# Optimization experiments

Measured on AMD Instinct MI355X. Metric: run time of the kernel, lower is better.

The kernel has to match this reference:

```python
import jax, jax.numpy as jnp
from jax import lax
import numpy as np

B = 2048; D_IN = 784; H = 256; N_OUT = 10

def setup_inputs() -> dict:
    key = jax.random.key(0)
    ks = jax.random.split(key, 12)
    return {
        "x": jax.random.uniform(ks[0], (B, D_IN), jnp.float32),
        "h1": jax.random.randint(ks[1], (B, H), 0, 2, jnp.int32),
        "h2": jax.random.randint(ks[2], (B, H), 0, 2, jnp.int32),
        "y": jax.random.randint(ks[3], (B, N_OUT), 0, 2, jnp.int32),
        "W1": jax.random.normal(ks[4], (D_IN, H), jnp.float32) * 0.05,
        "b1": jnp.zeros((H,), jnp.float32),
        "W2": jax.random.normal(ks[5], (H, H), jnp.float32) * 0.05,
        "b2": jnp.zeros((H,), jnp.float32),
        "Wout": jax.random.normal(ks[6], (H, N_OUT), jnp.float32) * 0.05,
        "bout": jnp.zeros((N_OUT,), jnp.float32),
        # pre-drawn per-node Bernoulli uniforms, shape [H, B] (scan axis first)
        "u1": jax.random.uniform(ks[7], (H, B), jnp.float32),
        "u2": jax.random.uniform(ks[8], (H, B), jnp.float32),
    }

def _sigmoid_ce(labels, logits):
    # tf.nn.sigmoid_cross_entropy_with_logits, numerically stable
    return jnp.maximum(logits, 0.0) - logits * labels + jnp.log1p(jnp.exp(-jnp.abs(logits)))

def _gibbs_layer(pv, cv, nv, W_in, b_in, W_out, b_out, u):
    """One layer of node-by-node Gibbs resampling.
    pv: [B, P] parents, cv: [B, H] current layer (old values),
    nv: [B, Hn] children, u: [H, B] uniforms. Returns (new cv [B,H], final child logits [B,Hn])."""
    parent_logits = pv @ W_in + b_in          # [B, H]; sigmoid(.) = prob_parents
    next_logits0 = cv @ W_out + b_out         # [B, Hn], recurrently updated

    def step(nl, xs):
        node, w_j, pl_j, u_j = xs             # [B], [Hn], [B], [B]
        nl0 = nl - node[:, None] * w_j[None, :]
        nl1 = nl + (1.0 - node)[:, None] * w_j[None, :]
        lp0 = -jnp.sum(_sigmoid_ce(nv, nl0), axis=-1)
        lp1 = -jnp.sum(_sigmoid_ce(nv, nl1), axis=-1)
        # prob = p1/(p1+p0) with p1 = sigm(pl)*exp(lp1), p0 = (1-sigm(pl))*exp(lp0)
        # == sigmoid(pl + lp1 - lp0)  (same math, stable form)
        prob = jax.nn.sigmoid(pl_j + lp1 - lp0)
        new = (u_j < prob).astype(jnp.float32)
        nl_new = jnp.where(new[:, None] > 0.5, nl1, nl0)
        return nl_new, new

    nl_fin, new_T = lax.scan(step, next_logits0, (cv.T, W_out, parent_logits.T, u))
    return new_T.T, nl_fin

def reference(x, h1, h2, y, W1, b1, W2, b2, Wout, bout, u1, u2):
    h1f = h1.astype(jnp.float32)
    h2f = h2.astype(jnp.float32)
    yf = y.astype(jnp.float32)
    # layer 0: parents=x, children=h2 (old values)
    h1_new, _ = _gibbs_layer(x, h1f, h2f, W1, b1, W2, b2, u1)
    # layer 1: parents=h1_new (already updated), children=y, out layer = output_layer
    h2_new, nl_fin = _gibbs_layer(h1_new, h2f, yf, W2, b2, Wout, bout, u2)
    # pack new states + final output-layer logits into one array [B, H+H+N_OUT]
    return jnp.concatenate([h1_new, h2_new, nl_fin], axis=1)
```

## Files before the change

kernel.cpp:

```cpp
#include <hip/hip_runtime.h>
#include <math.h>

#define NB   2048
#define DIN  784
#define HN   256
#define NOUT 10
#define OSTR (HN + HN + NOUT)

struct Smem {
  float4  sup[4][HN];
  double2 tab[65];
  float   scr[4][16 * 20];
  float   h2o[4][HN];
  float   h1n[4][HN];
  float   tmp[4][HN];
  float   yv [4][16];
};

__device__ __forceinline__ float np_expf(float xf) {
  float q = __fmul_rn(xf, 1.442695040888963f);
  q = __fadd_rn(q, 12582912.0f);
  q = __fsub_rn(q, 12582912.0f);
  float x = __builtin_fmaf(q, -6.93145752e-1f, xf);
  x = __builtin_fmaf(q, -1.42860677e-6f, x);
  float num = __builtin_fmaf(x, 5.082762527590693718096e-04f,
                                6.757896990527504603057e-03f);
  num = __builtin_fmaf(num, x, 5.114512081637298353406e-02f);
  num = __builtin_fmaf(num, x, 2.473615434895520810817e-01f);
  num = __builtin_fmaf(num, x, 7.257664613233124478488e-01f);
  num = __builtin_fmaf(num, x, 9.999999999980870924916e-01f);
  float den = __builtin_fmaf(x, 2.159509375685829852307e-02f,
                                -2.742335390411667452936e-01f);
  den = __builtin_fmaf(den, x, 1.0f);
  float r = __fdiv_rn(num, den);
  int qi = (int)q;
  return __fmul_rn(r, __int_as_float((qi + 127) << 23));
}

__device__ __forceinline__ float np_log1pf(float ef, const double2* __restrict__ tab) {
  if (ef < 0x1p-29f) return ef;
  double t  = 1.0 + (double)ef;
  double kd = rint(t * 64.0);
  int   idx = (int)kd - 64;
  double2 te = tab[idx];
  double c  = kd * 0.015625;
  double s  = (t - c) * te.y;
  double p  = fma(s, -1.0/6.0, 0.2);
  p = fma(p, s, -0.25);
  p = fma(p, s,  1.0/3.0);
  p = fma(p, s, -0.5);
  p = fma(p, s,  1.0);
  p = p * s;
  return (float)(te.x + p);
}

__device__ __forceinline__ float ce32(float l, float label, const double2* __restrict__ tab) {
  float t3 = __fsub_rn(fmaxf(l, 0.0f), __fmul_rn(l, label));
  return __fadd_rn(t3, np_log1pf(np_expf(-fabsf(l)), tab));
}

__device__ __forceinline__ bool decide(float u, float ez) {
  float w = __fadd_rn(1.0f, ez);
  float d = __builtin_fmaf(u, w, -1.0f);
  if (__builtin_expect(fabsf(d) < 1e-5f, 0)) {
    float prob = __fdiv_rn(1.0f, w);
    return u < prob;
  }
  return d < 0.0f;
}

template<int CTRL> __device__ __forceinline__ float dppx(float v) {
  return __int_as_float(__builtin_amdgcn_mov_dpp(__float_as_int(v), CTRL, 0xF, 0xF, true));
}
__device__ __forceinline__ float rdl(float v, int l) {
  return __int_as_float(__builtin_amdgcn_readlane(__float_as_int(v), l));
}

__device__ __forceinline__ float sum10(float c) {
  float c0 = rdl(c, 0), c1 = rdl(c, 1), c2 = rdl(c, 2), c3 = rdl(c, 3);
  float c4 = rdl(c, 4), c5 = rdl(c, 5), c6 = rdl(c, 6), c7 = rdl(c, 7);
  float c8 = rdl(c, 8), c9 = rdl(c, 9);
  float t = __fadd_rn(__fadd_rn(__fadd_rn(c0, c1), __fadd_rn(c2, c3)),
                      __fadd_rn(__fadd_rn(c4, c5), __fadd_rn(c6, c7)));
  t = __fadd_rn(t, c8);
  t = __fadd_rn(t, c9);
  return t;
}

__device__ __forceinline__ float fold256_lds(const float c[4], float* __restrict__ scrw,
                                             int idx, int g) {
  *reinterpret_cast<float4*>(scrw + idx * 20 + 4 * g) = make_float4(c[0], c[1], c[2], c[3]);
  const float4* rp = reinterpret_cast<const float4*>(scrw + idx * 20);
  float4 q0 = rp[0], q1 = rp[1], q2 = rp[2], q3 = rp[3];
  float r = q0.x;
  r = __fadd_rn(r, q0.y); r = __fadd_rn(r, q0.z); r = __fadd_rn(r, q0.w);
  r = __fadd_rn(r, q1.x); r = __fadd_rn(r, q1.y); r = __fadd_rn(r, q1.z); r = __fadd_rn(r, q1.w);
  r = __fadd_rn(r, q2.x); r = __fadd_rn(r, q2.y); r = __fadd_rn(r, q2.z); r = __fadd_rn(r, q2.w);
  r = __fadd_rn(r, q3.x); r = __fadd_rn(r, q3.y); r = __fadd_rn(r, q3.z); r = __fadd_rn(r, q3.w);
  r = __fadd_rn(r, dppx<0xB1>(r));
  r = __fadd_rn(r, dppx<0x4E>(r));
  float B0 = rdl(r, 0), B1 = rdl(r, 4), B2 = rdl(r, 8), B3 = rdl(r, 12);
  return __fadd_rn(__fadd_rn(B0, B1), __fadd_rn(B2, B3));
}

__device__ __forceinline__ float fast_sum256(float loc) {
  float r = loc;
  r = r + dppx<0xB1>(r);
  r = r + dppx<0x4E>(r);
  r = r + dppx<0x124>(r);
  r = r + dppx<0x128>(r);
  r = r + dppx<0x142>(r);
  r = r + dppx<0x143>(r);
  return rdl(r, 63);
}

__device__ __forceinline__ float lu_of(float u) {
  if (u < 1e-4f || u > 0.9999f) return __int_as_float(0x7FC00000);
  return __logf(u) - __logf(__fsub_rn(1.0f, u));
}

#define ZBAND 0.05f
#define LN2F  0.6931471805599453f

__global__ __launch_bounds__(256) void stoch_mlp(
    const float* __restrict__ x,  const int* __restrict__ h1,
    const int* __restrict__ h2,   const int* __restrict__ y,
    const float* __restrict__ W1, const float* __restrict__ b1,
    const float* __restrict__ W2, const float* __restrict__ b2,
    const float* __restrict__ Wo, const float* __restrict__ bo,
    const float* __restrict__ u1, const float* __restrict__ u2,
    float* __restrict__ out)
{
  __shared__ Smem sm;
  const int t    = threadIdx.x;
  const int lane = t & 63;
  const int wid  = t >> 6;
  const int b0   = blockIdx.x * 4;
  const int b    = b0 + wid;

  if (t < 65) {
    double c = (double)(t + 64) * 0.015625;
    sm.tab[t] = make_double2(log(c), 64.0 / (double)(t + 64));
  }
  for (int j = lane; j < HN; j += 64) sm.h2o[wid][j] = (float)h2[b * HN + j];
  if (lane < 16) sm.yv[wid][lane] = (lane < NOUT) ? (float)y[b * NOUT + lane] : 0.0f;
  {
    float a0 = 0.0f, a1 = 0.0f, a2 = 0.0f, a3 = 0.0f;
    const float* x0 = x + (size_t)b0 * DIN;
    float wk0 = W1[t];
    float wk1 = W1[HN + t];
    for (int k = 0; k < DIN; ++k) {
      int k2 = (k + 2 < DIN) ? (k + 2) : 0;
      float wk2 = W1[(size_t)k2 * HN + t];
      a0 = __builtin_fmaf(x0[k],           wk0, a0);
      a1 = __builtin_fmaf(x0[DIN   + k],   wk0, a1);
      a2 = __builtin_fmaf(x0[2*DIN + k],   wk0, a2);
      a3 = __builtin_fmaf(x0[3*DIN + k],   wk0, a3);
      wk0 = wk1; wk1 = wk2;
    }
    float bb = b1[t];
    float4 uv = *reinterpret_cast<const float4*>(u1 + (size_t)t * NB + b0);
    float n0 = (float)h1[(b0 + 0) * HN + t];
    float n1 = (float)h1[(b0 + 1) * HN + t];
    float n2 = (float)h1[(b0 + 2) * HN + t];
    float n3 = (float)h1[(b0 + 3) * HN + t];
    sm.sup[0][t] = make_float4(n0, uv.x, __fadd_rn(a0, bb), lu_of(uv.x));
    sm.sup[1][t] = make_float4(n1, uv.y, __fadd_rn(a1, bb), lu_of(uv.y));
    sm.sup[2][t] = make_float4(n2, uv.z, __fadd_rn(a2, bb), lu_of(uv.z));
    sm.sup[3][t] = make_float4(n3, uv.w, __fadd_rn(a3, bb), lu_of(uv.w));
  }
  __syncthreads();

  const double2* tab = sm.tab;
  float* scrw = &sm.scr[wid][0];

  {
    float acc[4] = {0.0f, 0.0f, 0.0f, 0.0f};
    for (int j = 0; j < HN; ++j) {
      float nodej = sm.sup[wid][j].x;
      float4 wf = *reinterpret_cast<const float4*>(W2 + (size_t)j * HN + 4*lane);
      acc[0] = __builtin_fmaf(nodej, wf.x, acc[0]);
      acc[1] = __builtin_fmaf(nodej, wf.y, acc[1]);
      acc[2] = __builtin_fmaf(nodej, wf.z, acc[2]);
      acc[3] = __builtin_fmaf(nodej, wf.w, acc[3]);
    }
    float4 bv = *reinterpret_cast<const float4*>(b2 + 4*lane);
    *reinterpret_cast<float4*>(&sm.tmp[wid][4*lane]) =
        make_float4(__fadd_rn(acc[0], bv.x), __fadd_rn(acc[1], bv.y),
                    __fadd_rn(acc[2], bv.z), __fadd_rn(acc[3], bv.w));
  }

  const int idx  = lane & 15;
  const int g    = lane >> 4;
  const int half = idx >> 3;
  const int jacc = idx & 7;
  const int kb   = half * 128 + (4 * g) * 8 + jacc;

  float nlv[4], nv[4];
  int   smk[4];
  #pragma unroll
  for (int i = 0; i < 4; ++i) {
    int k = kb + i * 8;
    nlv[i] = sm.tmp[wid][k];
    nv[i]  = sm.h2o[wid][k];
    smk[i] = (nv[i] != 0.0f) ? (int)0x80000000 : 0;
  }
  float S_c;
  {
    float ci[4];
    #pragma unroll
    for (int i = 0; i < 4; ++i) ci[i] = ce32(nlv[i], nv[i], tab);
    S_c = fold256_lds(ci, scrw, idx, g);
  }

  {
    float4 supC = sm.sup[wid][0];
    float4 supN = sm.sup[wid][1];
    float w0[4], w1[4];
    #pragma unroll
    for (int i = 0; i < 4; ++i) {
      w0[i] = W2[kb + i * 8];
      w1[i] = W2[(size_t)HN + kb + i * 8];
    }
    #pragma unroll 2
    for (int j = 0; j < HN; ++j) {
      int jn2 = (j + 2) & (HN - 1);
      float4 supN2 = sm.sup[wid][jn2];
      float wp[4];
      #pragma unroll
      for (int i = 0; i < 4; ++i) wp[i] = W2[(size_t)jn2 * HN + kb + i * 8];

      float node = supC.x, uj = supC.y, plj = supC.z, luj = supC.w;
      bool  nd   = (node != 0.0f);
      int ndm = nd ? (int)0x80000000 : 0;
      float fresh[4], t3[4], p[4];
      #pragma unroll
      for (int i = 0; i < 4; ++i) {
        float ws = __int_as_float(__float_as_int(w0[i]) ^ ndm);
        fresh[i] = __fadd_rn(nlv[i], ws);
        float sl = __int_as_float(__float_as_int(fresh[i]) ^ smk[i]);
        t3[i] = fmaxf(sl, 0.0f);
        p[i]  = __log2f(__fadd_rn(1.0f, __expf(-fabsf(fresh[i]))));
      }
      float T = (t3[0] + t3[1]) + (t3[2] + t3[3]);
      float P = (p[0]  + p[1])  + (p[2]  + p[3]);
      float F = fast_sum256(__builtin_fmaf(LN2F, P, T));
      float sgn = nd ? 1.0f : -1.0f;
      float z = __builtin_fmaf(F - S_c, sgn, plj);
      float d = z - luj;
      bool nw;
      if (__builtin_expect(!(fabsf(d) >= ZBAND), 0)) {
        float one_m = __fsub_rn(1.0f, node);
        float nl0[4], nl1[4], c0i[4], c1i[4];
        #pragma unroll
        for (int i = 0; i < 4; ++i) {
          nl0[i] = __fsub_rn(nlv[i], __fmul_rn(node,  w0[i]));
          nl1[i] = __fadd_rn(nlv[i], __fmul_rn(one_m, w0[i]));
          c0i[i] = ce32(nl0[i], nv[i], tab);
          c1i[i] = ce32(nl1[i], nv[i], tab);
        }
        float S0e = fold256_lds(c0i, scrw, idx, g);
        float S1e = fold256_lds(c1i, scrw, idx, g);
        float ze  = __fsub_rn(__fadd_rn(plj, -S1e), -S0e);
        nw  = decide(uj, np_expf(-ze));
        S_c = nw ? S1e : S0e;
        #pragma unroll
        for (int i = 0; i < 4; ++i) nlv[i] = nw ? nl1[i] : nl0[i];
      } else {
        nw = d > 0.0f;
        bool flip = (nw != nd);
        S_c = flip ? F : S_c;
        #pragma unroll
        for (int i = 0; i < 4; ++i) nlv[i] = flip ? fresh[i] : nlv[i];
      }
      if (lane == 0) sm.h1n[wid][j] = nw ? 1.0f : 0.0f;
      supC = supN; supN = supN2;
      #pragma unroll
      for (int i = 0; i < 4; ++i) { w0[i] = w1[i]; w1[i] = wp[i]; }
    }
  }

  {
    float acc[4] = {0.0f, 0.0f, 0.0f, 0.0f};
    for (int j = 0; j < HN; ++j) {
      float nodej = sm.h1n[wid][j];
      float4 wf = *reinterpret_cast<const float4*>(W2 + (size_t)j * HN + 4*lane);
      acc[0] = __builtin_fmaf(nodej, wf.x, acc[0]);
      acc[1] = __builtin_fmaf(nodej, wf.y, acc[1]);
      acc[2] = __builtin_fmaf(nodej, wf.z, acc[2]);
      acc[3] = __builtin_fmaf(nodej, wf.w, acc[3]);
    }
    float4 bv = *reinterpret_cast<const float4*>(b2 + 4*lane);
    float p2[4] = {__fadd_rn(acc[0], bv.x), __fadd_rn(acc[1], bv.y),
                   __fadd_rn(acc[2], bv.z), __fadd_rn(acc[3], bv.w)};
    #pragma unroll
    for (int i = 0; i < 4; ++i) {
      int j = 4 * lane + i;
      float u2v = u2[(size_t)j * NB + b];
      sm.sup[wid][j] = make_float4(sm.h2o[wid][j], u2v, p2[i], lu_of(u2v));
    }
  }

  float nvy = 0.0f, nlo = 0.0f;
  if (lane < NOUT) {
    nvy = sm.yv[wid][lane];
    float a = 0.0f;
    for (int j = 0; j < HN; ++j)
      a = __builtin_fmaf(sm.h2o[wid][j], Wo[j * NOUT + lane], a);
    nlo = __fadd_rn(a, bo[lane]);
  }
  float S_c1 = sum10((lane < NOUT) ? ce32(nlo, nvy, tab) : 0.0f);
  const int  syk  = (nvy != 0.0f) ? (int)0x80000000 : 0;
  const bool lact = (lane < NOUT);

  {
    float4 supC = sm.sup[wid][0];
    float4 supN = sm.sup[wid][1];
    float w0s = lact ? Wo[lane] : 0.0f;
    float w1s = lact ? Wo[NOUT + lane] : 0.0f;
    #pragma unroll 2
    for (int j = 0; j < HN; ++j) {
      int jn2 = (j + 2) & (HN - 1);
      float4 supN2 = sm.sup[wid][jn2];
      float wps = lact ? Wo[jn2 * NOUT + lane] : 0.0f;

      float node = supC.x, uj = supC.y, plj = supC.z, luj = supC.w;
      bool  nd   = (node != 0.0f);
      int ndm = nd ? (int)0x80000000 : 0;
      float ws = __int_as_float(__float_as_int(w0s) ^ ndm);
      float fresh = __fadd_rn(nlo, ws);
      float sl = __int_as_float(__float_as_int(fresh) ^ syk);
      float t3 = fmaxf(sl, 0.0f);
      float p  = __log2f(__fadd_rn(1.0f, __expf(-fabsf(fresh))));
      float loc = lact ? __builtin_fmaf(LN2F, p, t3) : 0.0f;
      float r = loc;
      r = r + dppx<0xB1>(r);
      r = r + dppx<0x4E>(r);
      r = r + dppx<0x124>(r);
      r = r + dppx<0x128>(r);
      float F  = rdl(r, 0);
      float sgn = nd ? 1.0f : -1.0f;
      float z = __builtin_fmaf(F - S_c1, sgn, plj);
      float d = z - luj;
      bool nw;
      if (__builtin_expect(!(fabsf(d) >= ZBAND), 0)) {
        float one_m = __fsub_rn(1.0f, node);
        float nl0 = __fsub_rn(nlo, __fmul_rn(node,  w0s));
        float nl1 = __fadd_rn(nlo, __fmul_rn(one_m, w0s));
        float c0 = lact ? ce32(nl0, nvy, tab) : 0.0f;
        float c1 = lact ? ce32(nl1, nvy, tab) : 0.0f;
        float S0e = sum10(c0);
        float S1e = sum10(c1);
        float ze  = __fsub_rn(__fadd_rn(plj, -S1e), -S0e);
        nw   = decide(uj, np_expf(-ze));
        S_c1 = nw ? S1e : S0e;
        nlo  = nw ? nl1 : nl0;
      } else {
        nw = d > 0.0f;
        bool flip = (nw != nd);
        S_c1 = flip ? F : S_c1;
        nlo  = flip ? fresh : nlo;
      }
      if (lane == 0) out[(size_t)b * OSTR + HN + j] = nw ? 1.0f : 0.0f;
      supC = supN; supN = supN2;
      w0s = w1s; w1s = wps;
    }
  }

  float* orow = out + (size_t)b * OSTR;
  for (int j = lane; j < HN; j += 64) orow[j] = sm.h1n[wid][j];
  if (lane < NOUT) orow[2*HN + lane] = nlo;
}

extern "C" void kernel_launch(void* const* d_in, const int* in_sizes, int n_in,
                              void* d_out, int out_size, void* d_ws, size_t ws_size,
                              hipStream_t stream) {
  const float* x  = (const float*)d_in[0];
  const int*   h1 = (const int*)  d_in[1];
  const int*   h2 = (const int*)  d_in[2];
  const int*   y  = (const int*)  d_in[3];
  const float* W1 = (const float*)d_in[4];
  const float* b1 = (const float*)d_in[5];
  const float* W2 = (const float*)d_in[6];
  const float* b2 = (const float*)d_in[7];
  const float* Wo = (const float*)d_in[8];
  const float* bo = (const float*)d_in[9];
  const float* u1 = (const float*)d_in[10];
  const float* u2 = (const float*)d_in[11];
  stoch_mlp<<<NB/4, 256, 0, stream>>>(x, h1, h2, y, W1, b1, W2, b2, Wo, bo, u1, u2,
                                      (float*)d_out);
}
```

Measured before the change: 318.6 us.

## Deepen load prefetch rings and fold node-sign into precomputed decision offset

Replaces the two-deep register prefetch of weights and per-node support data with 4- or 16-deep rotating buffers across the W1, W2, Wo and Gibbs-scan loops, with matching unrolls. The goal is to hide global and LDS load latency in the serial scans. It also precomputes a sign-folded q = ±(pl − logit(u)) per node, so the decision becomes (F − S) + q. It multiplies the four softplus arguments before taking one log2 instead of four. The deeper buffers raise register pressure, and the product-of-logs change slightly alters rounding near the decision band.

```diff
diff --git a/kernel.cpp b/kernel.cpp
--- a/kernel.cpp
+++ b/kernel.cpp
@@ -118,6 +118,11 @@
   if (u < 1e-4f || u > 0.9999f) return __int_as_float(0x7FC00000);
   return __logf(u) - __logf(__fsub_rn(1.0f, u));
 }
+__device__ __forceinline__ float q_of(float node, float pl, float u) {
+  float lu = lu_of(u);
+  float pq = __fsub_rn(pl, lu);
+  return (node != 0.0f) ? pq : -pq;
+}
 
 #define ZBAND 0.05f
 #define LN2F  0.6931471805599453f
@@ -147,16 +152,18 @@
   {
     float a0 = 0.0f, a1 = 0.0f, a2 = 0.0f, a3 = 0.0f;
     const float* x0 = x + (size_t)b0 * DIN;
-    float wk0 = W1[t];
-    float wk1 = W1[HN + t];
+    float wk[16];
+    #pragma unroll
+    for (int i = 0; i < 16; ++i) wk[i] = W1[(size_t)i * HN + t];
+    #pragma unroll 16
     for (int k = 0; k < DIN; ++k) {
-      int k2 = (k + 2 < DIN) ? (k + 2) : 0;
-      float wk2 = W1[(size_t)k2 * HN + t];
-      a0 = __builtin_fmaf(x0[k],           wk0, a0);
-      a1 = __builtin_fmaf(x0[DIN   + k],   wk0, a1);
-      a2 = __builtin_fmaf(x0[2*DIN + k],   wk0, a2);
-      a3 = __builtin_fmaf(x0[3*DIN + k],   wk0, a3);
-      wk0 = wk1; wk1 = wk2;
+      float w = wk[k & 15];
+      int kp = (k + 16 < DIN) ? (k + 16) : 0;
+      wk[k & 15] = W1[(size_t)kp * HN + t];
+      a0 = __builtin_fmaf(x0[k],           w, a0);
+      a1 = __builtin_fmaf(x0[DIN   + k],   w, a1);
+      a2 = __builtin_fmaf(x0[2*DIN + k],   w, a2);
+      a3 = __builtin_fmaf(x0[3*DIN + k],   w, a3);
     }
     float bb = b1[t];
     float4 uv = *reinterpret_cast<const float4*>(u1 + (size_t)t * NB + b0);
@@ -164,10 +171,12 @@
     float n1 = (float)h1[(b0 + 1) * HN + t];
     float n2 = (float)h1[(b0 + 2) * HN + t];
     float n3 = (float)h1[(b0 + 3) * HN + t];
-    sm.sup[0][t] = make_float4(n0, uv.x, __fadd_rn(a0, bb), lu_of(uv.x));
-    sm.sup[1][t] = make_float4(n1, uv.y, __fadd_rn(a1, bb), lu_of(uv.y));
-    sm.sup[2][t] = make_float4(n2, uv.z, __fadd_rn(a2, bb), lu_of(uv.z));
-    sm.sup[3][t] = make_float4(n3, uv.w, __fadd_rn(a3, bb), lu_of(uv.w));
+    float p0 = __fadd_rn(a0, bb), p1v = __fadd_rn(a1, bb);
+    float p2v = __fadd_rn(a2, bb), p3 = __fadd_rn(a3, bb);
+    sm.sup[0][t] = make_float4(n0, uv.x, p0,  q_of(n0, p0,  uv.x));
+    sm.sup[1][t] = make_float4(n1, uv.y, p1v, q_of(n1, p1v, uv.y));
+    sm.sup[2][t] = make_float4(n2, uv.z, p2v, q_of(n2, p2v, uv.z));
+    sm.sup[3][t] = make_float4(n3, uv.w, p3,  q_of(n3, p3,  uv.w));
   }
   __syncthreads();
 
@@ -176,9 +185,16 @@
 
   {
     float acc[4] = {0.0f, 0.0f, 0.0f, 0.0f};
+    float4 wb[4];
+    #pragma unroll
+    for (int i = 0; i < 4; ++i)
+      wb[i] = *reinterpret_cast<const float4*>(W2 + (size_t)i * HN + 4*lane);
+    #pragma unroll 4
     for (int j = 0; j < HN; ++j) {
+      float4 wf = wb[j & 3];
+      int jp = (j + 4) & (HN - 1);
+      wb[j & 3] = *reinterpret_cast<const float4*>(W2 + (size_t)jp * HN + 4*lane);
       float nodej = sm.sup[wid][j].x;
-      float4 wf = *reinterpret_cast<const float4*>(W2 + (size_t)j * HN + 4*lane);
       acc[0] = __builtin_fmaf(nodej, wf.x, acc[0]);
       acc[1] = __builtin_fmaf(nodej, wf.y, acc[1]);
       acc[2] = __builtin_fmaf(nodej, wf.z, acc[2]);
@@ -214,77 +230,82 @@
   }
 
   {
-    float4 supC = sm.sup[wid][0];
-    float4 supN = sm.sup[wid][1];
-    float w0[4], w1[4];
+    float4 sref[4];
+    float wv[4][4];
     #pragma unroll
     for (int i = 0; i < 4; ++i) {
-      w0[i] = W2[kb + i * 8];
-      w1[i] = W2[(size_t)HN + kb + i * 8];
-    }
-    #pragma unroll 2
+      sref[i] = sm.sup[wid][i];
+      #pragma unroll
+      for (int c = 0; c < 4; ++c) wv[i][c] = W2[(size_t)i * HN + kb + c * 8];
+    }
+    #pragma unroll 4
     for (int j = 0; j < HN; ++j) {
-      int jn2 = (j + 2) & (HN - 1);
-      float4 supN2 = sm.sup[wid][jn2];
-      float wp[4];
+      const int sl = j & 3;
+      float4 sc = sref[sl];
+      float wc[4];
       #pragma unroll
-      for (int i = 0; i < 4; ++i) wp[i] = W2[(size_t)jn2 * HN + kb + i * 8];
-
-      float node = supC.x, uj = supC.y, plj = supC.z, luj = supC.w;
+      for (int c = 0; c < 4; ++c) wc[c] = wv[sl][c];
+      int jp = (j + 4) & (HN - 1);
+      sref[sl] = sm.sup[wid][jp];
+      #pragma unroll
+      for (int c = 0; c < 4; ++c) wv[sl][c] = W2[(size_t)jp * HN + kb + c * 8];
+
+      float node = sc.x, uj = sc.y, plj = sc.z, qj = sc.w;
       bool  nd   = (node != 0.0f);
       int ndm = nd ? (int)0x80000000 : 0;
-      float fresh[4], t3[4], p[4];
+      float fresh[4], t3v[4], av[4];
       #pragma unroll
-      for (int i = 0; i < 4; ++i) {
-        float ws = __int_as_float(__float_as_int(w0[i]) ^ ndm);
-        fresh[i] = __fadd_rn(nlv[i], ws);
-        float sl = __int_as_float(__float_as_int(fresh[i]) ^ smk[i]);
-        t3[i] = fmaxf(sl, 0.0f);
-        p[i]  = __log2f(__fadd_rn(1.0f, __expf(-fabsf(fresh[i]))));
+      for (int c = 0; c < 4; ++c) {
+        float ws = __int_as_float(__float_as_int(wc[c]) ^ ndm);
+        fresh[c] = __fadd_rn(nlv[c], ws);
+        float sl2 = __int_as_float(__float_as_int(fresh[c]) ^ smk[c]);
+        t3v[c] = fmaxf(sl2, 0.0f);
+        av[c]  = __fadd_rn(1.0f, __expf(-fabsf(fresh[c])));
       }
-      float T = (t3[0] + t3[1]) + (t3[2] + t3[3]);
-      float P = (p[0]  + p[1])  + (p[2]  + p[3]);
-      float F = fast_sum256(__builtin_fmaf(LN2F, P, T));
-      float sgn = nd ? 1.0f : -1.0f;
-      float z = __builtin_fmaf(F - S_c, sgn, plj);
-      float d = z - luj;
-      bool nw;
-      if (__builtin_expect(!(fabsf(d) >= ZBAND), 0)) {
+      float T    = (t3v[0] + t3v[1]) + (t3v[2] + t3v[3]);
+      float prod = (av[0] * av[1]) * (av[2] * av[3]);
+      float F = fast_sum256(__builtin_fmaf(LN2F, __log2f(prod), T));
+      float dd = (F - S_c) + qj;
+      if (__builtin_expect(!(fabsf(dd) >= ZBAND), 0)) {
         float one_m = __fsub_rn(1.0f, node);
         float nl0[4], nl1[4], c0i[4], c1i[4];
         #pragma unroll
-        for (int i = 0; i < 4; ++i) {
-          nl0[i] = __fsub_rn(nlv[i], __fmul_rn(node,  w0[i]));
-          nl1[i] = __fadd_rn(nlv[i], __fmul_rn(one_m, w0[i]));
-          c0i[i] = ce32(nl0[i], nv[i], tab);
-          c1i[i] = ce32(nl1[i], nv[i], tab);
+        for (int c = 0; c < 4; ++c) {
+          nl0[c] = __fsub_rn(nlv[c], __fmul_rn(node,  wc[c]));
+          nl1[c] = __fadd_rn(nlv[c], __fmul_rn(one_m, wc[c]));
+          c0i[c] = ce32(nl0[c], nv[c], tab);
+          c1i[c] = ce32(nl1[c], nv[c], tab);
         }
         float S0e = fold256_lds(c0i, scrw, idx, g);
         float S1e = fold256_lds(c1i, scrw, idx, g);
         float ze  = __fsub_rn(__fadd_rn(plj, -S1e), -S0e);
-        nw  = decide(uj, np_expf(-ze));
+        bool nw = decide(uj, np_expf(-ze));
         S_c = nw ? S1e : S0e;
         #pragma unroll
-        for (int i = 0; i < 4; ++i) nlv[i] = nw ? nl1[i] : nl0[i];
+        for (int c = 0; c < 4; ++c) nlv[c] = nw ? nl1[c] : nl0[c];
+        if (lane == 0) sm.h1n[wid][j] = nw ? 1.0f : 0.0f;
       } else {
-        nw = d > 0.0f;
-        bool flip = (nw != nd);
+        bool flip = dd < 0.0f;
         S_c = flip ? F : S_c;
         #pragma unroll
-        for (int i = 0; i < 4; ++i) nlv[i] = flip ? fresh[i] : nlv[i];
+        for (int c = 0; c < 4; ++c) nlv[c] = flip ? fresh[c] : nlv[c];
+        if (lane == 0) sm.h1n[wid][j] = flip ? __fsub_rn(1.0f, node) : node;
       }
-      if (lane == 0) sm.h1n[wid][j] = nw ? 1.0f : 0.0f;
-      supC = supN; supN = supN2;
-      #pragma unroll
-      for (int i = 0; i < 4; ++i) { w0[i] = w1[i]; w1[i] = wp[i]; }
     }
   }
 
   {
     float acc[4] = {0.0f, 0.0f, 0.0f, 0.0f};
+    float4 wb[4];
+    #pragma unroll
+    for (int i = 0; i < 4; ++i)
+      wb[i] = *reinterpret_cast<const float4*>(W2 + (size_t)i * HN + 4*lane);
+    #pragma unroll 4
     for (int j = 0; j < HN; ++j) {
+      float4 wf = wb[j & 3];
+      int jp = (j + 4) & (HN - 1);
+      wb[j & 3] = *reinterpret_cast<const float4*>(W2 + (size_t)jp * HN + 4*lane);
       float nodej = sm.h1n[wid][j];
-      float4 wf = *reinterpret_cast<const float4*>(W2 + (size_t)j * HN + 4*lane);
       acc[0] = __builtin_fmaf(nodej, wf.x, acc[0]);
       acc[1] = __builtin_fmaf(nodej, wf.y, acc[1]);
       acc[2] = __builtin_fmaf(nodej, wf.z, acc[2]);
@@ -293,44 +314,62 @@
     float4 bv = *reinterpret_cast<const float4*>(b2 + 4*lane);
     float p2[4] = {__fadd_rn(acc[0], bv.x), __fadd_rn(acc[1], bv.y),
                    __fadd_rn(acc[2], bv.z), __fadd_rn(acc[3], bv.w)};
+    float u2v[4];
+    #pragma unroll
+    for (int i = 0; i < 4; ++i) u2v[i] = u2[(size_t)(4*lane + i) * NB + b];
     #pragma unroll
     for (int i = 0; i < 4; ++i) {
       int j = 4 * lane + i;
-      float u2v = u2[(size_t)j * NB + b];
-      sm.sup[wid][j] = make_float4(sm.h2o[wid][j], u2v, p2[i], lu_of(u2v));
-    }
-  }
-
-  float nvy = 0.0f, nlo = 0.0f;
-  if (lane < NOUT) {
-    nvy = sm.yv[wid][lane];
+      float nodej = sm.h2o[wid][j];
+      sm.sup[wid][j] = make_float4(nodej, u2v[i], p2[i], q_of(nodej, p2[i], u2v[i]));
+    }
+  }
+
+  const bool lact = (lane < NOUT);
+  float nvy = lact ? sm.yv[wid][lane] : 0.0f;
+  float nlo = 0.0f;
+  {
     float a = 0.0f;
-    for (int j = 0; j < HN; ++j)
-      a = __builtin_fmaf(sm.h2o[wid][j], Wo[j * NOUT + lane], a);
-    nlo = __fadd_rn(a, bo[lane]);
-  }
-  float S_c1 = sum10((lane < NOUT) ? ce32(nlo, nvy, tab) : 0.0f);
-  const int  syk  = (nvy != 0.0f) ? (int)0x80000000 : 0;
-  const bool lact = (lane < NOUT);
-
-  {
-    float4 supC = sm.sup[wid][0];
-    float4 supN = sm.sup[wid][1];
-    float w0s = lact ? Wo[lane] : 0.0f;
-    float w1s = lact ? Wo[NOUT + lane] : 0.0f;
-    #pragma unroll 2
+    float wr[4];
+    #pragma unroll
+    for (int i = 0; i < 4; ++i) wr[i] = lact ? Wo[i * NOUT + lane] : 0.0f;
+    #pragma unroll 4
     for (int j = 0; j < HN; ++j) {
-      int jn2 = (j + 2) & (HN - 1);
-      float4 supN2 = sm.sup[wid][jn2];
-      float wps = lact ? Wo[jn2 * NOUT + lane] : 0.0f;
-
-      float node = supC.x, uj = supC.y, plj = supC.z, luj = supC.w;
+      float wvv = wr[j & 3];
+      int jp = (j + 4) & (HN - 1);
+      wr[j & 3] = lact ? Wo[jp * NOUT + lane] : 0.0f;
+      a = __builtin_fmaf(sm.h2o[wid][j], wvv, a);
+    }
+    float bov = lact ? bo[lane] : 0.0f;
+    nlo = __fadd_rn(a, bov);
+  }
+  float S_c1 = sum10(lact ? ce32(nlo, nvy, tab) : 0.0f);
+  const int syk = (nvy != 0.0f) ? (int)0x80000000 : 0;
+
+  {
+    float4 sref[4];
+    float wos[4];
+    #pragma unroll
+    for (int i = 0; i < 4; ++i) {
+      sref[i] = sm.sup[wid][i];
+      wos[i]  = lact ? Wo[i * NOUT + lane] : 0.0f;
+    }
+    #pragma unroll 4
+    for (int j = 0; j < HN; ++j) {
+      const int sl = j & 3;
+      float4 sc = sref[sl];
+      float w0s = wos[sl];
+      int jp = (j + 4) & (HN - 1);
+      sref[sl] = sm.sup[wid][jp];
+      wos[sl]  = lact ? Wo[jp * NOUT + lane] : 0.0f;
+
+      float node = sc.x, uj = sc.y, plj = sc.z, qj = sc.w;
       bool  nd   = (node != 0.0f);
       int ndm = nd ? (int)0x80000000 : 0;
       float ws = __int_as_float(__float_as_int(w0s) ^ ndm);
       float fresh = __fadd_rn(nlo, ws);
-      float sl = __int_as_float(__float_as_int(fresh) ^ syk);
-      float t3 = fmaxf(sl, 0.0f);
+      float sl2 = __int_as_float(__float_as_int(fresh) ^ syk);
+      float t3 = fmaxf(sl2, 0.0f);
       float p  = __log2f(__fadd_rn(1.0f, __expf(-fabsf(fresh))));
       float loc = lact ? __builtin_fmaf(LN2F, p, t3) : 0.0f;
       float r = loc;
@@ -339,11 +378,8 @@
       r = r + dppx<0x124>(r);
       r = r + dppx<0x128>(r);
       float F  = rdl(r, 0);
-      float sgn = nd ? 1.0f : -1.0f;
-      float z = __builtin_fmaf(F - S_c1, sgn, plj);
-      float d = z - luj;
-      bool nw;
-      if (__builtin_expect(!(fabsf(d) >= ZBAND), 0)) {
+      float dd = (F - S_c1) + qj;
+      if (__builtin_expect(!(fabsf(dd) >= ZBAND), 0)) {
         float one_m = __fsub_rn(1.0f, node);
         float nl0 = __fsub_rn(nlo, __fmul_rn(node,  w0s));
         float nl1 = __fadd_rn(nlo, __fmul_rn(one_m, w0s));
@@ -352,18 +388,16 @@
         float S0e = sum10(c0);
         float S1e = sum10(c1);
         float ze  = __fsub_rn(__fadd_rn(plj, -S1e), -S0e);
-        nw   = decide(uj, np_expf(-ze));
+        bool nw = decide(uj, np_expf(-ze));
         S_c1 = nw ? S1e : S0e;
         nlo  = nw ? nl1 : nl0;
+        if (lane == 0) out[(size_t)b * OSTR + HN + j] = nw ? 1.0f : 0.0f;
       } else {
-        nw = d > 0.0f;
-        bool flip = (nw != nd);
+        bool flip = dd < 0.0f;
         S_c1 = flip ? F : S_c1;
         nlo  = flip ? fresh : nlo;
+        if (lane == 0) out[(size_t)b * OSTR + HN + j] = flip ? __fsub_rn(1.0f, node) : node;
       }
-      if (lane == 0) out[(size_t)b * OSTR + HN + j] = nw ? 1.0f : 0.0f;
-      supC = supN; supN = supN2;
-      w0s = w1s; w1s = wps;
     }
   }
 
```

Result: slower. 334.0 us (+4.8%).
